# Performance work log

Hardware: AMD Instinct MI355X
Metric: run time of the kernel (lower is better)

The kernel has to match this reference:

```python
import jax, jax.numpy as jnp
import numpy as np
import math

B, C, T = 8, 256, 8192
G = 128          # group_size
QK = 128         # query_key_dim
HID = 512        # int(input_dim * expansion_factor)


def laplace_attn(x):
    mu = math.sqrt(0.5)
    std = math.sqrt(0.25 * math.pi)
    return (1.0 + jax.lax.erf((x - mu) / (std * math.sqrt(2.0)))) * 0.5


def setup_inputs() -> dict:
    key = jax.random.key(0)
    ks = jax.random.split(key, 12)
    s = 0.02
    q = jax.random.normal(ks[0], (B, C, T), jnp.float32)
    k = jax.random.normal(ks[1], (B, C, T), jnp.float32)
    v = jax.random.normal(ks[2], (B, C, T), jnp.float32)
    masks = jax.random.randint(ks[3], (B, 1, T), 0, 2).astype(jnp.float32)
    Wg = jax.random.normal(ks[4], (C, HID), jnp.float32) * s
    bg = jnp.zeros((HID,), jnp.float32)
    Wv = jax.random.normal(ks[5], (C, HID), jnp.float32) * s
    bv = jnp.zeros((HID,), jnp.float32)
    Wqk = jax.random.normal(ks[6], (C, QK), jnp.float32) * s
    bqk = jnp.zeros((QK,), jnp.float32)
    gamma = 1.0 + jax.random.normal(ks[7], (4, QK), jnp.float32) * s
    beta = jnp.zeros((4, QK), jnp.float32)
    Wo = jax.random.normal(ks[8], (HID, C), jnp.float32) * s
    bo = jnp.zeros((C,), jnp.float32)
    return {"q": q, "k": k, "v": v, "masks": masks,
            "Wg": Wg, "bg": bg, "Wv": Wv, "bv": bv,
            "Wqk": Wqk, "bqk": bqk, "gamma": gamma, "beta": beta,
            "Wo": Wo, "bo": bo}


def reference(q, k, v, masks, Wg, bg, Wv, bv, Wqk, bqk, gamma, beta, Wo, bo):
    # gen_key_padding_mask: batches whose mask is all-zero are reset to 1
    all_zero = jnp.sum(masks, axis=(1, 2)) == 0.0            # [B]
    masks = jnp.where(all_zero[:, None, None], 1.0, masks)    # [B,1,T]
    kpm = masks[:, 0, :] == 0.0                                # [B,T] True where mask==0

    # InstanceNorm1d (no affine): normalize q over the T axis per (b, c)
    mu = jnp.mean(q, axis=-1, keepdims=True)
    var = jnp.var(q, axis=-1, keepdims=True)
    qn = (q - mu) / jnp.sqrt(var + 1e-5)

    x = jnp.transpose(qn, (0, 2, 1))   # [B,T,C]
    vt = jnp.transpose(v, (0, 2, 1))   # [B,T,C]

    gate = jax.nn.silu(x @ Wg + bg)    # [B,T,HID]
    vh = jax.nn.silu(vt @ Wv + bv)     # [B,T,HID]
    qk = jax.nn.silu(x @ Wqk + bqk)    # [B,T,QK]

    # OffsetScale with 4 heads -> quad_q, lin_q, quad_k, lin_k
    qk4 = qk[..., None, :] * gamma + beta              # [B,T,4,QK]
    quad_q, lin_q, quad_k, lin_k = (qk4[..., i, :] for i in range(4))

    # masked_fill(~lin_mask, 0): zero lin_k where kpm is False (source semantics)
    lin_k = jnp.where(kpm[..., None], lin_k, 0.0)

    # T is a multiple of G, so padding_to_multiple_of(n, g) == 0
    ng = T // G
    grp = lambda t: t.reshape(B, ng, G, t.shape[-1])
    qq, lq, qkk, lk, vg = map(grp, (quad_q, lin_q, quad_k, lin_k, vh))
    kpm_g = kpm.reshape(B, ng, 1, G)                   # [B,g,1,j]

    # quadratic (local, per-group) attention
    sim = jnp.einsum('bgid,bgjd->bgij', qq, qkk) / G
    attn = laplace_attn(sim)
    attn = jnp.where(kpm_g, attn, 0.0)                 # masked_fill(~kpm, 0)
    quad_out = jnp.einsum('bgij,bgje->bgie', attn, vg)

    # linear (global) attention, non-causal, per-group context
    lin_kv = jnp.einsum('bgnd,bgne->bgde', lk, vg) / T
    lin_out = jnp.einsum('bgnd,bgde->bgne', lq, lin_kv)

    out = gate * (quad_out + lin_out).reshape(B, T, HID)
    out = (out @ Wo + bo).transpose(0, 2, 1)           # [B,C,T]
    return out * masks
```

## Files before the change

### kernel.cpp

```cpp
#include <hip/hip_runtime.h>
#include <stdint.h>

#define B_ 8
#define C_ 256
#define T_ 8192
#define G_ 128
#define QK_ 128
#define HID_ 512
#define NG_ 64

typedef __attribute__((ext_vector_type(8))) short bf16x8;
typedef __attribute__((ext_vector_type(4))) short s16x4;
typedef __attribute__((ext_vector_type(4))) float f32x4;

__device__ __forceinline__ float b2f(short s){
  union { float f; unsigned u; } v; v.u = ((unsigned)(unsigned short)s) << 16; return v.f;
}
__device__ __forceinline__ short f2b(float f){
  union { float f; unsigned u; } v; v.f = f;
  unsigned r = (v.u + 0x7FFFu + ((v.u >> 16) & 1u)) >> 16;
  return (short)r;
}
__device__ __forceinline__ float silu_f(float x){ return x / (1.0f + expf(-x)); }
__device__ __forceinline__ float laplace_f(float x){
  return 0.5f * (1.0f + erff((x - 0.70710678f) * 0.79788456f));
}
__device__ __forceinline__ f32x4 mfma16(bf16x8 a, bf16x8 b, f32x4 c){
  return __builtin_amdgcn_mfma_f32_16x16x32_bf16(a, b, c, 0, 0, 0);
}

__global__ void kw(const float* __restrict__ Wg, const float* __restrict__ Wv,
                   const float* __restrict__ Wqk, const float* __restrict__ Wo,
                   short* __restrict__ wgT, short* __restrict__ wvT,
                   short* __restrict__ wqkT, short* __restrict__ woT){
  int idx = blockIdx.x * 256 + threadIdx.x;
  int stride = gridDim.x * 256;
  for (int i = idx; i < C_ * HID_; i += stride){
    int c = i / HID_, e = i % HID_;
    wgT[e * C_ + c] = f2b(Wg[i]);
    wvT[e * C_ + c] = f2b(Wv[i]);
  }
  for (int i = idx; i < C_ * QK_; i += stride){
    int c = i / QK_, d = i % QK_;
    wqkT[d * C_ + c] = f2b(Wqk[i]);
  }
  for (int i = idx; i < HID_ * C_; i += stride){
    int e = i / C_, c = i % C_;
    woT[c * HID_ + e] = f2b(Wo[i]);
  }
}

__global__ void k0(const float* __restrict__ masks, float* __restrict__ m_eff,
                   float* __restrict__ kpmf){
  int b = blockIdx.x, tid = threadIdx.x;
  __shared__ float red[256];
  float s = 0.f;
  for (int t = tid; t < T_; t += 256) s += masks[b * T_ + t];
  red[tid] = s; __syncthreads();
  for (int k = 128; k > 0; k >>= 1){ if (tid < k) red[tid] += red[tid + k]; __syncthreads(); }
  bool az = (red[0] == 0.0f);
  for (int t = tid; t < T_; t += 256){
    float m = az ? 1.0f : masks[b * T_ + t];
    m_eff[b * T_ + t] = m;
    kpmf[b * T_ + t] = (m == 0.0f) ? 1.0f : 0.0f;
  }
}

__global__ void k1(const float* __restrict__ q, float* __restrict__ mu, float* __restrict__ rstd){
  int bc = blockIdx.x, tid = threadIdx.x;
  const float* row = q + (size_t)bc * T_;
  float s = 0.f, ss = 0.f;
  for (int t = tid * 4; t < T_; t += 256 * 4){
    float4 v = *(const float4*)(row + t);
    s += v.x + v.y + v.z + v.w;
    ss += v.x * v.x + v.y * v.y + v.z * v.z + v.w * v.w;
  }
  __shared__ float r1[256], r2[256];
  r1[tid] = s; r2[tid] = ss; __syncthreads();
  for (int k = 128; k > 0; k >>= 1){
    if (tid < k){ r1[tid] += r1[tid + k]; r2[tid] += r2[tid + k]; }
    __syncthreads();
  }
  if (tid == 0){
    float m = r1[0] / (float)T_;
    float var = r2[0] / (float)T_ - m * m;
    mu[bc] = m;
    rstd[bc] = rsqrtf(var + 1e-5f);
  }
}

__launch_bounds__(512)
__global__ void k2(const float* __restrict__ q, const float* __restrict__ v,
                   const float* __restrict__ mu, const float* __restrict__ rstd,
                   const short* __restrict__ wgT, const short* __restrict__ wvT,
                   const short* __restrict__ wqkT,
                   const float* __restrict__ bg, const float* __restrict__ bqk,
                   const float* __restrict__ bv,
                   const float* __restrict__ gamma, const float* __restrict__ beta,
                   const float* __restrict__ kpmf,
                   short* __restrict__ qqb, short* __restrict__ lqb,
                   short* __restrict__ qkkb, short* __restrict__ lkb,
                   short* __restrict__ gate, short* __restrict__ vhT){
  __shared__ __align__(16) short xlds[64 * 264];
  __shared__ __align__(16) short stage[9728];
  int blk = blockIdx.x;
  int b = blk >> 7, tile = blk & 127;
  int t0 = tile * 64;
  int tid = threadIdx.x;
  int w = tid >> 6, lane = tid & 63, lr = lane & 15, lg = lane >> 4;
  int wm = w >> 2, wn = w & 3;
  int i0w = wm * 32, n0w = wn * 32;

  {
    int cr = tid >> 4, tf = (tid & 15) * 4;
    #pragma unroll
    for (int it = 0; it < 8; ++it){
      int c = it * 32 + cr;
      float4 val = *(const float4*)(q + (size_t)(b * C_ + c) * T_ + t0 + tf);
      float m = mu[b * C_ + c], rs = rstd[b * C_ + c];
      xlds[(tf + 0) * 264 + c] = f2b((val.x - m) * rs);
      xlds[(tf + 1) * 264 + c] = f2b((val.y - m) * rs);
      xlds[(tf + 2) * 264 + c] = f2b((val.z - m) * rs);
      xlds[(tf + 3) * 264 + c] = f2b((val.w - m) * rs);
    }
  }
  __syncthreads();

  for (int p = 0; p < 5; ++p){
    const short* wt = (p < 4) ? (wgT + p * 128 * C_) : wqkT;
    const float* bias = (p < 4) ? (bg + p * 128) : bqk;
    f32x4 acc[2][2];
    #pragma unroll
    for (int mi = 0; mi < 2; ++mi)
      #pragma unroll
      for (int ni = 0; ni < 2; ++ni) acc[mi][ni] = (f32x4){0.f, 0.f, 0.f, 0.f};
    #pragma unroll
    for (int ks = 0; ks < 8; ++ks){
      int kb = ks * 32 + lg * 8;
      bf16x8 a[2], bb[2];
      #pragma unroll
      for (int mi = 0; mi < 2; ++mi)
        a[mi] = *(const bf16x8*)&xlds[(i0w + mi * 16 + lr) * 264 + kb];
      #pragma unroll
      for (int ni = 0; ni < 2; ++ni)
        bb[ni] = *(const bf16x8*)(wt + (n0w + ni * 16 + lr) * C_ + kb);
      #pragma unroll
      for (int mi = 0; mi < 2; ++mi)
        #pragma unroll
        for (int ni = 0; ni < 2; ++ni)
          acc[mi][ni] = mfma16(a[mi], bb[ni], acc[mi][ni]);
    }
    if (p < 4){
      #pragma unroll
      for (int ni = 0; ni < 2; ++ni){
        float bvv = bias[n0w + ni * 16 + lr];
        #pragma unroll
        for (int mi = 0; mi < 2; ++mi)
          #pragma unroll
          for (int r = 0; r < 4; ++r){
            int i = i0w + mi * 16 + lg * 4 + r;
            stage[i * 136 + n0w + ni * 16 + lr] = f2b(silu_f(acc[mi][ni][r] + bvv));
          }
      }
      __syncthreads();
      int row = tid >> 3, l8 = tid & 7;
      short* dst = gate + (size_t)(b * T_ + t0 + row) * HID_ + p * 128 + l8 * 16;
      *(uint4*)(dst) = *(const uint4*)&stage[row * 136 + l8 * 16];
      *(uint4*)(dst + 8) = *(const uint4*)&stage[row * 136 + l8 * 16 + 8];
      __syncthreads();
    } else {
      float sreg[2][2][4];
      float kpv[2][4];
      #pragma unroll
      for (int ni = 0; ni < 2; ++ni){
        float bvv = bias[n0w + ni * 16 + lr];
        #pragma unroll
        for (int mi = 0; mi < 2; ++mi)
          #pragma unroll
          for (int r = 0; r < 4; ++r)
            sreg[mi][ni][r] = silu_f(acc[mi][ni][r] + bvv);
      }
      #pragma unroll
      for (int mi = 0; mi < 2; ++mi)
        #pragma unroll
        for (int r = 0; r < 4; ++r)
          kpv[mi][r] = kpmf[b * T_ + t0 + i0w + mi * 16 + lg * 4 + r];
      short* hd[4] = {qqb, lqb, qkkb, lkb};
      for (int h = 0; h < 4; ++h){
        float gv[2], bvv2[2];
        #pragma unroll
        for (int ni = 0; ni < 2; ++ni){
          int n = n0w + ni * 16 + lr;
          gv[ni] = gamma[h * QK_ + n];
          bvv2[ni] = beta[h * QK_ + n];
        }
        #pragma unroll
        for (int mi = 0; mi < 2; ++mi)
          #pragma unroll
          for (int ni = 0; ni < 2; ++ni)
            #pragma unroll
            for (int r = 0; r < 4; ++r){
              float val = sreg[mi][ni][r] * gv[ni] + bvv2[ni];
              if (h == 3) val *= kpv[mi][r];
              stage[(i0w + mi * 16 + lg * 4 + r) * 136 + n0w + ni * 16 + lr] = f2b(val);
            }
        __syncthreads();
        int row = tid >> 3, l8 = tid & 7;
        short* dst = hd[h] + (size_t)(b * T_ + t0 + row) * QK_ + l8 * 16;
        *(uint4*)(dst) = *(const uint4*)&stage[row * 136 + l8 * 16];
        *(uint4*)(dst + 8) = *(const uint4*)&stage[row * 136 + l8 * 16 + 8];
        __syncthreads();
      }
    }
  }

  {
    int cr = tid >> 4, tf = (tid & 15) * 4;
    #pragma unroll
    for (int it = 0; it < 8; ++it){
      int c = it * 32 + cr;
      float4 val = *(const float4*)(v + (size_t)(b * C_ + c) * T_ + t0 + tf);
      xlds[(tf + 0) * 264 + c] = f2b(val.x);
      xlds[(tf + 1) * 264 + c] = f2b(val.y);
      xlds[(tf + 2) * 264 + c] = f2b(val.z);
      xlds[(tf + 3) * 264 + c] = f2b(val.w);
    }
  }
  __syncthreads();
  for (int p = 0; p < 4; ++p){
    const short* wt = wvT + p * 128 * C_;
    f32x4 acc[2][2];
    #pragma unroll
    for (int mi = 0; mi < 2; ++mi)
      #pragma unroll
      for (int ni = 0; ni < 2; ++ni) acc[mi][ni] = (f32x4){0.f, 0.f, 0.f, 0.f};
    #pragma unroll
    for (int ks = 0; ks < 8; ++ks){
      int kb = ks * 32 + lg * 8;
      bf16x8 a[2], bb[2];
      #pragma unroll
      for (int mi = 0; mi < 2; ++mi)
        a[mi] = *(const bf16x8*)&xlds[(i0w + mi * 16 + lr) * 264 + kb];
      #pragma unroll
      for (int ni = 0; ni < 2; ++ni)
        bb[ni] = *(const bf16x8*)(wt + (n0w + ni * 16 + lr) * C_ + kb);
      #pragma unroll
      for (int mi = 0; mi < 2; ++mi)
        #pragma unroll
        for (int ni = 0; ni < 2; ++ni)
          acc[mi][ni] = mfma16(a[mi], bb[ni], acc[mi][ni]);
    }
    #pragma unroll
    for (int ni = 0; ni < 2; ++ni){
      int n = n0w + ni * 16 + lr;
      float bvv = bv[p * 128 + n];
      #pragma unroll
      for (int mi = 0; mi < 2; ++mi){
        int ib = i0w + mi * 16 + lg * 4;
        s16x4 pk;
        #pragma unroll
        for (int r = 0; r < 4; ++r) pk[r] = f2b(silu_f(acc[mi][ni][r] + bvv));
        *(s16x4*)&stage[n * 72 + ib] = pk;
      }
    }
    __syncthreads();
    int row = tid >> 2, l4 = tid & 3;
    short* dst = vhT + (size_t)(b * HID_ + p * 128 + row) * T_ + t0 + l4 * 16;
    *(uint4*)(dst) = *(const uint4*)&stage[row * 72 + l4 * 16];
    *(uint4*)(dst + 8) = *(const uint4*)&stage[row * 72 + l4 * 16 + 8];
    __syncthreads();
  }
}

__launch_bounds__(512)
__global__ void k3(const short* __restrict__ qqb, const short* __restrict__ qkkb,
                   const short* __restrict__ lqb, const short* __restrict__ lkb,
                   const short* __restrict__ gate, const short* __restrict__ vhT,
                   const short* __restrict__ woT,
                   const float* __restrict__ kpmf, const float* __restrict__ m_eff,
                   const float* __restrict__ bo, float* __restrict__ out){
  __shared__ __align__(16) short slotA[128 * 136];
  __shared__ __align__(16) short slotB[128 * 136];
  __shared__ __align__(16) short slotC[128 * 136];
  int blk = blockIdx.x;
  int b = blk >> 6, grp = blk & 63;
  int t0 = grp * G_;
  int tid = threadIdx.x;
  int w = tid >> 6, lane = tid & 63, lr = lane & 15, lg = lane >> 4;
  int wm = w >> 2, wn = w & 3;
  int i0w = wm * 64;
  int j0w = wn * 32;
  int e0w = wn * 32;
  int d0w = wn * 32;
  int c0w = wn * 64;

  {
    const short* src = lkb + (size_t)(b * T_ + t0) * QK_;
    int d4 = (tid & 31) * 4;
    #pragma unroll
    for (int rep = 0; rep < 8; ++rep){
      int n = rep * 16 + (tid >> 5);
      s16x4 vv = *(const s16x4*)(src + n * QK_ + d4);
      #pragma unroll
      for (int r = 0; r < 4; ++r) slotC[(d4 + r) * 136 + n] = vv[r];
    }
  }

  {
    const short* qqp = qqb + (size_t)(b * T_ + t0) * QK_;
    const short* qkkp = qkkb + (size_t)(b * T_ + t0) * QK_;
    f32x4 sacc[4][2];
    #pragma unroll
    for (int mi = 0; mi < 4; ++mi)
      #pragma unroll
      for (int ni = 0; ni < 2; ++ni) sacc[mi][ni] = (f32x4){0.f, 0.f, 0.f, 0.f};
    #pragma unroll
    for (int ks = 0; ks < 4; ++ks){
      int kb = ks * 32 + lg * 8;
      bf16x8 a[4], bb[2];
      #pragma unroll
      for (int mi = 0; mi < 4; ++mi)
        a[mi] = *(const bf16x8*)(qqp + (i0w + mi * 16 + lr) * QK_ + kb);
      #pragma unroll
      for (int ni = 0; ni < 2; ++ni)
        bb[ni] = *(const bf16x8*)(qkkp + (j0w + ni * 16 + lr) * QK_ + kb);
      #pragma unroll
      for (int mi = 0; mi < 4; ++mi)
        #pragma unroll
        for (int ni = 0; ni < 2; ++ni)
          sacc[mi][ni] = mfma16(a[mi], bb[ni], sacc[mi][ni]);
    }
    #pragma unroll
    for (int ni = 0; ni < 2; ++ni){
      int j = j0w + ni * 16 + lr;
      float kp = kpmf[b * T_ + t0 + j];
      #pragma unroll
      for (int mi = 0; mi < 4; ++mi)
        #pragma unroll
        for (int r = 0; r < 4; ++r){
          int i = i0w + mi * 16 + lg * 4 + r;
          float s = sacc[mi][ni][r] * (1.0f / 128.0f);
          slotB[i * 136 + j] = f2b(laplace_f(s) * kp);
        }
    }
  }
  __syncthreads();

  f32x4 oacc[4][4];
  #pragma unroll
  for (int mi = 0; mi < 4; ++mi)
    #pragma unroll
    for (int ni = 0; ni < 4; ++ni) oacc[mi][ni] = (f32x4){0.f, 0.f, 0.f, 0.f};

  const short* lqp = lqb + (size_t)(b * T_ + t0) * QK_;

  for (int cN = 0; cN < 4; ++cN){
    int e0 = cN * 128;
    const short* vhp = vhT + (size_t)(b * HID_ + e0) * T_ + t0;

    f32x4 pacc[4][2];
    #pragma unroll
    for (int mi = 0; mi < 4; ++mi)
      #pragma unroll
      for (int ni = 0; ni < 2; ++ni) pacc[mi][ni] = (f32x4){0.f, 0.f, 0.f, 0.f};
    #pragma unroll
    for (int ks = 0; ks < 4; ++ks){
      int jb = ks * 32 + lg * 8;
      bf16x8 a[4], bb[2];
      #pragma unroll
      for (int mi = 0; mi < 4; ++mi)
        a[mi] = *(const bf16x8*)&slotB[(i0w + mi * 16 + lr) * 136 + jb];
      #pragma unroll
      for (int ni = 0; ni < 2; ++ni)
        bb[ni] = *(const bf16x8*)(vhp + (size_t)(e0w + ni * 16 + lr) * T_ + jb);
      #pragma unroll
      for (int mi = 0; mi < 4; ++mi)
        #pragma unroll
        for (int ni = 0; ni < 2; ++ni)
          pacc[mi][ni] = mfma16(a[mi], bb[ni], pacc[mi][ni]);
    }

    {
      f32x4 lacc[4][2];
      #pragma unroll
      for (int mi = 0; mi < 4; ++mi)
        #pragma unroll
        for (int ni = 0; ni < 2; ++ni) lacc[mi][ni] = (f32x4){0.f, 0.f, 0.f, 0.f};
      #pragma unroll
      for (int ks = 0; ks < 4; ++ks){
        int jb = ks * 32 + lg * 8;
        bf16x8 a[4], bb[2];
        #pragma unroll
        for (int mi = 0; mi < 4; ++mi)
          a[mi] = *(const bf16x8*)(vhp + (size_t)(i0w + mi * 16 + lr) * T_ + jb);
        #pragma unroll
        for (int ni = 0; ni < 2; ++ni)
          bb[ni] = *(const bf16x8*)&slotC[(d0w + ni * 16 + lr) * 136 + jb];
        #pragma unroll
        for (int mi = 0; mi < 4; ++mi)
          #pragma unroll
          for (int ni = 0; ni < 2; ++ni)
            lacc[mi][ni] = mfma16(a[mi], bb[ni], lacc[mi][ni]);
      }
      #pragma unroll
      for (int mi = 0; mi < 4; ++mi)
        #pragma unroll
        for (int ni = 0; ni < 2; ++ni){
          int d = d0w + ni * 16 + lr;
          #pragma unroll
          for (int r = 0; r < 4; ++r){
            int e = i0w + mi * 16 + lg * 4 + r;
            slotA[e * 136 + d] = f2b(lacc[mi][ni][r] * (1.0f / 8192.0f));
          }
        }
    }
    __syncthreads();

    #pragma unroll
    for (int ks = 0; ks < 4; ++ks){
      int db = ks * 32 + lg * 8;
      bf16x8 a[4], bb[2];
      #pragma unroll
      for (int mi = 0; mi < 4; ++mi)
        a[mi] = *(const bf16x8*)(lqp + (i0w + mi * 16 + lr) * QK_ + db);
      #pragma unroll
      for (int ni = 0; ni < 2; ++ni)
        bb[ni] = *(const bf16x8*)&slotA[(e0w + ni * 16 + lr) * 136 + db];
      #pragma unroll
      for (int mi = 0; mi < 4; ++mi)
        #pragma unroll
        for (int ni = 0; ni < 2; ++ni)
          pacc[mi][ni] = mfma16(a[mi], bb[ni], pacc[mi][ni]);
    }
    __syncthreads();

    {
      const short* gp = gate + (size_t)(b * T_ + t0) * HID_ + e0;
      int row = tid >> 2, l4 = tid & 3;
      #pragma unroll
      for (int jj = 0; jj < 4; ++jj)
        *(uint4*)&slotA[row * 136 + l4 * 32 + jj * 8] =
            *(const uint4*)(gp + (size_t)row * HID_ + l4 * 32 + jj * 8);
    }
    __syncthreads();

    #pragma unroll
    for (int mi = 0; mi < 4; ++mi)
      #pragma unroll
      for (int ni = 0; ni < 2; ++ni){
        int e = e0w + ni * 16 + lr;
        #pragma unroll
        for (int r = 0; r < 4; ++r){
          int i = i0w + mi * 16 + lg * 4 + r;
          int idx = i * 136 + e;
          slotA[idx] = f2b(b2f(slotA[idx]) * pacc[mi][ni][r]);
        }
      }
    __syncthreads();

    #pragma unroll
    for (int ks = 0; ks < 4; ++ks){
      int eb = ks * 32 + lg * 8;
      bf16x8 a[4], bb[4];
      #pragma unroll
      for (int mi = 0; mi < 4; ++mi)
        a[mi] = *(const bf16x8*)&slotA[(i0w + mi * 16 + lr) * 136 + eb];
      #pragma unroll
      for (int ni = 0; ni < 4; ++ni)
        bb[ni] = *(const bf16x8*)(woT + (size_t)(c0w + ni * 16 + lr) * HID_ + e0 + eb);
      #pragma unroll
      for (int mi = 0; mi < 4; ++mi)
        #pragma unroll
        for (int ni = 0; ni < 4; ++ni)
          oacc[mi][ni] = mfma16(a[mi], bb[ni], oacc[mi][ni]);
    }
    __syncthreads();
  }

  float* fstage = (float*)(void*)slotA;
  for (int cp = 0; cp < 4; ++cp){
    if (wn == cp){
      #pragma unroll
      for (int mi = 0; mi < 4; ++mi)
        #pragma unroll
        for (int ni = 0; ni < 4; ++ni){
          int cc = ni * 16 + lr;
          int ib = i0w + mi * 16 + lg * 4;
          *(f32x4*)&fstage[cc * 132 + ib] = oacc[mi][ni];
        }
    }
    __syncthreads();
    int crow = tid >> 3, l8 = tid & 7;
    int c = cp * 64 + crow;
    float bov = bo[c];
    float* orow = out + (size_t)(b * C_ + c) * T_ + t0;
    const float* mrow = m_eff + (size_t)b * T_ + t0;
    #pragma unroll
    for (int jj = 0; jj < 4; ++jj){
      int toff = l8 * 16 + jj * 4;
      float4 a = *(const float4*)&fstage[crow * 132 + toff];
      float4 m = *(const float4*)(mrow + toff);
      float4 o;
      o.x = (a.x + bov) * m.x; o.y = (a.y + bov) * m.y;
      o.z = (a.z + bov) * m.z; o.w = (a.w + bov) * m.w;
      *(float4*)(orow + toff) = o;
    }
    __syncthreads();
  }
}

extern "C" void kernel_launch(void* const* d_in, const int* in_sizes, int n_in,
                              void* d_out, int out_size, void* d_ws, size_t ws_size,
                              hipStream_t stream) {
  const float* q     = (const float*)d_in[0];
  const float* v     = (const float*)d_in[2];
  const float* masks = (const float*)d_in[3];
  const float* Wg    = (const float*)d_in[4];
  const float* bg    = (const float*)d_in[5];
  const float* Wv    = (const float*)d_in[6];
  const float* bv    = (const float*)d_in[7];
  const float* Wqk   = (const float*)d_in[8];
  const float* bqk   = (const float*)d_in[9];
  const float* gamma = (const float*)d_in[10];
  const float* beta  = (const float*)d_in[11];
  const float* Wo    = (const float*)d_in[12];
  const float* bo    = (const float*)d_in[13];
  float* out = (float*)d_out;

  char* ws = (char*)d_ws;
  size_t o = 0;
  auto nxt = [&](size_t bytes) -> char* {
    char* p = ws + o;
    o += (bytes + 255) & ~(size_t)255;
    return p;
  };
  short* wgT   = (short*)nxt((size_t)HID_ * C_ * 2);
  short* wvT   = (short*)nxt((size_t)HID_ * C_ * 2);
  short* wqkT  = (short*)nxt((size_t)QK_ * C_ * 2);
  short* woT   = (short*)nxt((size_t)C_ * HID_ * 2);
  float* muW   = (float*)nxt((size_t)B_ * C_ * 4);
  float* rstdW = (float*)nxt((size_t)B_ * C_ * 4);
  float* m_eff = (float*)nxt((size_t)B_ * T_ * 4);
  float* kpmf  = (float*)nxt((size_t)B_ * T_ * 4);
  short* qqb   = (short*)nxt((size_t)B_ * T_ * QK_ * 2);
  short* lqb   = (short*)nxt((size_t)B_ * T_ * QK_ * 2);
  short* qkkb  = (short*)nxt((size_t)B_ * T_ * QK_ * 2);
  short* lkb   = (short*)nxt((size_t)B_ * T_ * QK_ * 2);
  short* gateW = (short*)nxt((size_t)B_ * T_ * HID_ * 2);
  short* vhT   = (short*)nxt((size_t)B_ * HID_ * T_ * 2);
  (void)in_sizes; (void)n_in; (void)out_size; (void)ws_size;

  kw<<<dim3(512), dim3(256), 0, stream>>>(Wg, Wv, Wqk, Wo, wgT, wvT, wqkT, woT);
  k0<<<dim3(B_), dim3(256), 0, stream>>>(masks, m_eff, kpmf);
  k1<<<dim3(B_ * C_), dim3(256), 0, stream>>>(q, muW, rstdW);
  k2<<<dim3(B_ * (T_ / 64)), dim3(512), 0, stream>>>(q, v, muW, rstdW, wgT, wvT, wqkT,
                                                     bg, bqk, bv, gamma, beta, kpmf,
                                                     qqb, lqb, qkkb, lkb, gateW, vhT);
  k3<<<dim3(B_ * NG_), dim3(512), 0, stream>>>(qqb, qkkb, lqb, lkb, gateW, vhT, woT,
                                               kpmf, m_eff, bo, out);
}
```

Baseline: 563.5 us.

## Split projection kernel into transpose pre-pass and 128-row projection kernels

Replaces the monolithic projection kernel with three kernels. kA normalizes q and converts q and v to bf16 in time-major layout. kB computes gate and qk with 128-row tiles and writes lin_k already transposed. kC computes the v projection into vhT, which reuses the xT workspace. Because lin_k arrives pre-transposed, the attention kernel no longer needs its LDS staging buffer, which cuts its shared-memory footprint, and silu switches to the fast __expf. The cost is an extra round trip of the bf16 transposed q/v through global memory, extra launches, and large LDS use per block in kB/kC.

Result: slower. 630.7 us (+11.9%).

```diff
diff --git a/kernel.cpp b/kernel.cpp
--- a/kernel.cpp
+++ b/kernel.cpp
@@ -21,7 +21,7 @@
   unsigned r = (v.u + 0x7FFFu + ((v.u >> 16) & 1u)) >> 16;
   return (short)r;
 }
-__device__ __forceinline__ float silu_f(float x){ return x / (1.0f + expf(-x)); }
+__device__ __forceinline__ float silu_f(float x){ return x / (1.0f + __expf(-x)); }
 __device__ __forceinline__ float laplace_f(float x){
   return 0.5f * (1.0f + erff((x - 0.70710678f) * 0.79788456f));
 }
@@ -89,199 +89,323 @@
   }
 }
 
+__global__ void kA(const float* __restrict__ q, const float* __restrict__ v,
+                   const float* __restrict__ mu, const float* __restrict__ rstd,
+                   short* __restrict__ xT, short* __restrict__ vT){
+  __shared__ __align__(16) short lds[64 * 72];
+  int blk = blockIdx.x;
+  int b = blk >> 9;
+  int rem = blk & 511;
+  int t0 = (rem >> 2) * 64;
+  int c0 = (rem & 3) * 64;
+  int tid = threadIdx.x;
+  int f = (tid & 15) * 4;
+  int crb = tid >> 4;
+
+  #pragma unroll
+  for (int it = 0; it < 4; ++it){
+    int cr = crb + it * 16;
+    int gc = b * C_ + c0 + cr;
+    float4 val = *(const float4*)(q + (size_t)gc * T_ + t0 + f);
+    float m = mu[gc], rs = rstd[gc];
+    lds[(f + 0) * 72 + cr] = f2b((val.x - m) * rs);
+    lds[(f + 1) * 72 + cr] = f2b((val.y - m) * rs);
+    lds[(f + 2) * 72 + cr] = f2b((val.z - m) * rs);
+    lds[(f + 3) * 72 + cr] = f2b((val.w - m) * rs);
+  }
+  __syncthreads();
+  {
+    int t = tid >> 2, l4 = tid & 3;
+    *(uint4*)(xT + (size_t)(b * T_ + t0 + t) * C_ + c0 + l4 * 16) =
+        *(const uint4*)&lds[t * 72 + l4 * 16];
+    *(uint4*)(xT + (size_t)(b * T_ + t0 + t) * C_ + c0 + l4 * 16 + 8) =
+        *(const uint4*)&lds[t * 72 + l4 * 16 + 8];
+  }
+  __syncthreads();
+
+  #pragma unroll
+  for (int it = 0; it < 4; ++it){
+    int cr = crb + it * 16;
+    int gc = b * C_ + c0 + cr;
+    float4 val = *(const float4*)(v + (size_t)gc * T_ + t0 + f);
+    lds[(f + 0) * 72 + cr] = f2b(val.x);
+    lds[(f + 1) * 72 + cr] = f2b(val.y);
+    lds[(f + 2) * 72 + cr] = f2b(val.z);
+    lds[(f + 3) * 72 + cr] = f2b(val.w);
+  }
+  __syncthreads();
+  {
+    int t = tid >> 2, l4 = tid & 3;
+    *(uint4*)(vT + (size_t)(b * T_ + t0 + t) * C_ + c0 + l4 * 16) =
+        *(const uint4*)&lds[t * 72 + l4 * 16];
+    *(uint4*)(vT + (size_t)(b * T_ + t0 + t) * C_ + c0 + l4 * 16 + 8) =
+        *(const uint4*)&lds[t * 72 + l4 * 16 + 8];
+  }
+}
+
 __launch_bounds__(512)
-__global__ void k2(const float* __restrict__ q, const float* __restrict__ v,
-                   const float* __restrict__ mu, const float* __restrict__ rstd,
-                   const short* __restrict__ wgT, const short* __restrict__ wvT,
-                   const short* __restrict__ wqkT,
+__global__ void kB(const short* __restrict__ xT,
+                   const short* __restrict__ wgT, const short* __restrict__ wqkT,
                    const float* __restrict__ bg, const float* __restrict__ bqk,
-                   const float* __restrict__ bv,
                    const float* __restrict__ gamma, const float* __restrict__ beta,
                    const float* __restrict__ kpmf,
+                   short* __restrict__ gate,
                    short* __restrict__ qqb, short* __restrict__ lqb,
-                   short* __restrict__ qkkb, short* __restrict__ lkb,
-                   short* __restrict__ gate, short* __restrict__ vhT){
-  __shared__ __align__(16) short xlds[64 * 264];
-  __shared__ __align__(16) short stage[9728];
+                   short* __restrict__ qkkb, short* __restrict__ lkT){
+  __shared__ __align__(16) short xs[128 * 264];
+  __shared__ __align__(16) short st[128 * 136];
   int blk = blockIdx.x;
-  int b = blk >> 7, tile = blk & 127;
-  int t0 = tile * 64;
+  int b = blk >> 6, tile = blk & 63;
+  int t0 = tile * 128;
   int tid = threadIdx.x;
   int w = tid >> 6, lane = tid & 63, lr = lane & 15, lg = lane >> 4;
   int wm = w >> 2, wn = w & 3;
-  int i0w = wm * 32, n0w = wn * 32;
+  int m0 = wm * 64, n0 = wn * 32;
 
   {
-    int cr = tid >> 4, tf = (tid & 15) * 4;
-    #pragma unroll
-    for (int it = 0; it < 8; ++it){
-      int c = it * 32 + cr;
-      float4 val = *(const float4*)(q + (size_t)(b * C_ + c) * T_ + t0 + tf);
-      float m = mu[b * C_ + c], rs = rstd[b * C_ + c];
-      xlds[(tf + 0) * 264 + c] = f2b((val.x - m) * rs);
-      xlds[(tf + 1) * 264 + c] = f2b((val.y - m) * rs);
-      xlds[(tf + 2) * 264 + c] = f2b((val.z - m) * rs);
-      xlds[(tf + 3) * 264 + c] = f2b((val.w - m) * rs);
+    const short* src = xT + (size_t)(b * T_ + t0) * C_;
+    int r = tid >> 4, c16 = (tid & 15) * 16;
+    #pragma unroll
+    for (int it = 0; it < 4; ++it){
+      int row = r + it * 32;
+      *(uint4*)&xs[row * 264 + c16]     = *(const uint4*)(src + (size_t)row * C_ + c16);
+      *(uint4*)&xs[row * 264 + c16 + 8] = *(const uint4*)(src + (size_t)row * C_ + c16 + 8);
     }
   }
   __syncthreads();
 
-  for (int p = 0; p < 5; ++p){
-    const short* wt = (p < 4) ? (wgT + p * 128 * C_) : wqkT;
-    const float* bias = (p < 4) ? (bg + p * 128) : bqk;
-    f32x4 acc[2][2];
-    #pragma unroll
-    for (int mi = 0; mi < 2; ++mi)
+  for (int p = 0; p < 4; ++p){
+    f32x4 acc[4][2];
+    #pragma unroll
+    for (int mi = 0; mi < 4; ++mi)
       #pragma unroll
       for (int ni = 0; ni < 2; ++ni) acc[mi][ni] = (f32x4){0.f, 0.f, 0.f, 0.f};
     #pragma unroll
     for (int ks = 0; ks < 8; ++ks){
       int kb = ks * 32 + lg * 8;
-      bf16x8 a[2], bb[2];
-      #pragma unroll
-      for (int mi = 0; mi < 2; ++mi)
-        a[mi] = *(const bf16x8*)&xlds[(i0w + mi * 16 + lr) * 264 + kb];
+      bf16x8 a[4], bb[2];
+      #pragma unroll
+      for (int mi = 0; mi < 4; ++mi)
+        a[mi] = *(const bf16x8*)&xs[(m0 + mi * 16 + lr) * 264 + kb];
       #pragma unroll
       for (int ni = 0; ni < 2; ++ni)
-        bb[ni] = *(const bf16x8*)(wt + (n0w + ni * 16 + lr) * C_ + kb);
-      #pragma unroll
-      for (int mi = 0; mi < 2; ++mi)
+        bb[ni] = *(const bf16x8*)(wgT + (size_t)(p * 128 + n0 + ni * 16 + lr) * C_ + kb);
+      #pragma unroll
+      for (int mi = 0; mi < 4; ++mi)
         #pragma unroll
         for (int ni = 0; ni < 2; ++ni)
           acc[mi][ni] = mfma16(a[mi], bb[ni], acc[mi][ni]);
     }
-    if (p < 4){
+    #pragma unroll
+    for (int ni = 0; ni < 2; ++ni){
+      int e = p * 128 + n0 + ni * 16 + lr;
+      float bvv = bg[e];
+      #pragma unroll
+      for (int mi = 0; mi < 4; ++mi)
+        #pragma unroll
+        for (int r = 0; r < 4; ++r)
+          st[(m0 + mi * 16 + lg * 4 + r) * 136 + n0 + ni * 16 + lr] =
+              f2b(silu_f(acc[mi][ni][r] + bvv));
+    }
+    __syncthreads();
+    {
+      int row = tid >> 2, l4 = tid & 3;
+      short* dst = gate + (size_t)(b * T_ + t0 + row) * HID_ + p * 128 + l4 * 32;
+      const short* srcs = &st[row * 136 + l4 * 32];
+      #pragma unroll
+      for (int jj = 0; jj < 4; ++jj)
+        *(uint4*)(dst + jj * 8) = *(const uint4*)(srcs + jj * 8);
+    }
+    __syncthreads();
+  }
+
+  {
+    f32x4 acc[4][2];
+    #pragma unroll
+    for (int mi = 0; mi < 4; ++mi)
+      #pragma unroll
+      for (int ni = 0; ni < 2; ++ni) acc[mi][ni] = (f32x4){0.f, 0.f, 0.f, 0.f};
+    #pragma unroll
+    for (int ks = 0; ks < 8; ++ks){
+      int kb = ks * 32 + lg * 8;
+      bf16x8 a[4], bb[2];
+      #pragma unroll
+      for (int mi = 0; mi < 4; ++mi)
+        a[mi] = *(const bf16x8*)&xs[(m0 + mi * 16 + lr) * 264 + kb];
+      #pragma unroll
+      for (int ni = 0; ni < 2; ++ni)
+        bb[ni] = *(const bf16x8*)(wqkT + (size_t)(n0 + ni * 16 + lr) * C_ + kb);
+      #pragma unroll
+      for (int mi = 0; mi < 4; ++mi)
+        #pragma unroll
+        for (int ni = 0; ni < 2; ++ni)
+          acc[mi][ni] = mfma16(a[mi], bb[ni], acc[mi][ni]);
+    }
+    float sreg[4][2][4];
+    #pragma unroll
+    for (int ni = 0; ni < 2; ++ni){
+      float bvv = bqk[n0 + ni * 16 + lr];
+      #pragma unroll
+      for (int mi = 0; mi < 4; ++mi)
+        #pragma unroll
+        for (int r = 0; r < 4; ++r)
+          sreg[mi][ni][r] = silu_f(acc[mi][ni][r] + bvv);
+    }
+    short* hd[3] = {qqb, lqb, qkkb};
+    for (int h = 0; h < 3; ++h){
       #pragma unroll
       for (int ni = 0; ni < 2; ++ni){
-        float bvv = bias[n0w + ni * 16 + lr];
-        #pragma unroll
-        for (int mi = 0; mi < 2; ++mi)
+        int d = n0 + ni * 16 + lr;
+        float gv = gamma[h * QK_ + d], bt = beta[h * QK_ + d];
+        #pragma unroll
+        for (int mi = 0; mi < 4; ++mi)
           #pragma unroll
-          for (int r = 0; r < 4; ++r){
-            int i = i0w + mi * 16 + lg * 4 + r;
-            stage[i * 136 + n0w + ni * 16 + lr] = f2b(silu_f(acc[mi][ni][r] + bvv));
-          }
+          for (int r = 0; r < 4; ++r)
+            st[(m0 + mi * 16 + lg * 4 + r) * 136 + d] = f2b(sreg[mi][ni][r] * gv + bt);
       }
       __syncthreads();
-      int row = tid >> 3, l8 = tid & 7;
-      short* dst = gate + (size_t)(b * T_ + t0 + row) * HID_ + p * 128 + l8 * 16;
-      *(uint4*)(dst) = *(const uint4*)&stage[row * 136 + l8 * 16];
-      *(uint4*)(dst + 8) = *(const uint4*)&stage[row * 136 + l8 * 16 + 8];
+      {
+        int row = tid >> 2, l4 = tid & 3;
+        short* dst = hd[h] + (size_t)(b * T_ + t0 + row) * QK_ + l4 * 32;
+        const short* srcs = &st[row * 136 + l4 * 32];
+        #pragma unroll
+        for (int jj = 0; jj < 4; ++jj)
+          *(uint4*)(dst + jj * 8) = *(const uint4*)(srcs + jj * 8);
+      }
       __syncthreads();
-    } else {
-      float sreg[2][2][4];
-      float kpv[2][4];
-      #pragma unroll
-      for (int ni = 0; ni < 2; ++ni){
-        float bvv = bias[n0w + ni * 16 + lr];
-        #pragma unroll
-        for (int mi = 0; mi < 2; ++mi)
-          #pragma unroll
-          for (int r = 0; r < 4; ++r)
-            sreg[mi][ni][r] = silu_f(acc[mi][ni][r] + bvv);
-      }
-      #pragma unroll
-      for (int mi = 0; mi < 2; ++mi)
-        #pragma unroll
-        for (int r = 0; r < 4; ++r)
-          kpv[mi][r] = kpmf[b * T_ + t0 + i0w + mi * 16 + lg * 4 + r];
-      short* hd[4] = {qqb, lqb, qkkb, lkb};
-      for (int h = 0; h < 4; ++h){
-        float gv[2], bvv2[2];
-        #pragma unroll
-        for (int ni = 0; ni < 2; ++ni){
-          int n = n0w + ni * 16 + lr;
-          gv[ni] = gamma[h * QK_ + n];
-          bvv2[ni] = beta[h * QK_ + n];
-        }
-        #pragma unroll
-        for (int mi = 0; mi < 2; ++mi)
-          #pragma unroll
-          for (int ni = 0; ni < 2; ++ni)
-            #pragma unroll
-            for (int r = 0; r < 4; ++r){
-              float val = sreg[mi][ni][r] * gv[ni] + bvv2[ni];
-              if (h == 3) val *= kpv[mi][r];
-              stage[(i0w + mi * 16 + lg * 4 + r) * 136 + n0w + ni * 16 + lr] = f2b(val);
-            }
-        __syncthreads();
-        int row = tid >> 3, l8 = tid & 7;
-        short* dst = hd[h] + (size_t)(b * T_ + t0 + row) * QK_ + l8 * 16;
-        *(uint4*)(dst) = *(const uint4*)&stage[row * 136 + l8 * 16];
-        *(uint4*)(dst + 8) = *(const uint4*)&stage[row * 136 + l8 * 16 + 8];
-        __syncthreads();
-      }
     }
   }
 
   {
-    int cr = tid >> 4, tf = (tid & 15) * 4;
-    #pragma unroll
-    for (int it = 0; it < 8; ++it){
-      int c = it * 32 + cr;
-      float4 val = *(const float4*)(v + (size_t)(b * C_ + c) * T_ + t0 + tf);
-      xlds[(tf + 0) * 264 + c] = f2b(val.x);
-      xlds[(tf + 1) * 264 + c] = f2b(val.y);
-      xlds[(tf + 2) * 264 + c] = f2b(val.z);
-      xlds[(tf + 3) * 264 + c] = f2b(val.w);
-    }
-  }
-  __syncthreads();
-  for (int p = 0; p < 4; ++p){
-    const short* wt = wvT + p * 128 * C_;
-    f32x4 acc[2][2];
-    #pragma unroll
-    for (int mi = 0; mi < 2; ++mi)
+    f32x4 acc[4][2];
+    #pragma unroll
+    for (int mi = 0; mi < 4; ++mi)
       #pragma unroll
       for (int ni = 0; ni < 2; ++ni) acc[mi][ni] = (f32x4){0.f, 0.f, 0.f, 0.f};
     #pragma unroll
     for (int ks = 0; ks < 8; ++ks){
       int kb = ks * 32 + lg * 8;
-      bf16x8 a[2], bb[2];
-      #pragma unroll
-      for (int mi = 0; mi < 2; ++mi)
-        a[mi] = *(const bf16x8*)&xlds[(i0w + mi * 16 + lr) * 264 + kb];
+      bf16x8 a[4], bb[2];
+      #pragma unroll
+      for (int mi = 0; mi < 4; ++mi)
+        a[mi] = *(const bf16x8*)(wqkT + (size_t)(m0 + mi * 16 + lr) * C_ + kb);
       #pragma unroll
       for (int ni = 0; ni < 2; ++ni)
-        bb[ni] = *(const bf16x8*)(wt + (n0w + ni * 16 + lr) * C_ + kb);
-      #pragma unroll
-      for (int mi = 0; mi < 2; ++mi)
+        bb[ni] = *(const bf16x8*)&xs[(n0 + ni * 16 + lr) * 264 + kb];
+      #pragma unroll
+      for (int mi = 0; mi < 4; ++mi)
         #pragma unroll
         for (int ni = 0; ni < 2; ++ni)
           acc[mi][ni] = mfma16(a[mi], bb[ni], acc[mi][ni]);
     }
-    #pragma unroll
-    for (int ni = 0; ni < 2; ++ni){
-      int n = n0w + ni * 16 + lr;
-      float bvv = bv[p * 128 + n];
-      #pragma unroll
-      for (int mi = 0; mi < 2; ++mi){
-        int ib = i0w + mi * 16 + lg * 4;
-        s16x4 pk;
-        #pragma unroll
-        for (int r = 0; r < 4; ++r) pk[r] = f2b(silu_f(acc[mi][ni][r] + bvv));
-        *(s16x4*)&stage[n * 72 + ib] = pk;
+    float kp[2];
+    #pragma unroll
+    for (int ni = 0; ni < 2; ++ni)
+      kp[ni] = kpmf[b * T_ + t0 + n0 + ni * 16 + lr];
+    #pragma unroll
+    for (int mi = 0; mi < 4; ++mi)
+      #pragma unroll
+      for (int r = 0; r < 4; ++r){
+        int d = m0 + mi * 16 + lg * 4 + r;
+        float bvv = bqk[d];
+        float gv = gamma[3 * QK_ + d], bt = beta[3 * QK_ + d];
+        #pragma unroll
+        for (int ni = 0; ni < 2; ++ni){
+          float val = (silu_f(acc[mi][ni][r] + bvv) * gv + bt) * kp[ni];
+          st[d * 136 + n0 + ni * 16 + lr] = f2b(val);
+        }
       }
-    }
-    __syncthreads();
-    int row = tid >> 2, l4 = tid & 3;
-    short* dst = vhT + (size_t)(b * HID_ + p * 128 + row) * T_ + t0 + l4 * 16;
-    *(uint4*)(dst) = *(const uint4*)&stage[row * 72 + l4 * 16];
-    *(uint4*)(dst + 8) = *(const uint4*)&stage[row * 72 + l4 * 16 + 8];
+    __syncthreads();
+    {
+      int row = tid >> 2, l4 = tid & 3;
+      short* dst = lkT + (size_t)(b * QK_ + row) * T_ + t0 + l4 * 32;
+      const short* srcs = &st[row * 136 + l4 * 32];
+      #pragma unroll
+      for (int jj = 0; jj < 4; ++jj)
+        *(uint4*)(dst + jj * 8) = *(const uint4*)(srcs + jj * 8);
+    }
+  }
+}
+
+__launch_bounds__(512)
+__global__ void kC(const short* __restrict__ vT, const short* __restrict__ wvT,
+                   const float* __restrict__ bv, short* __restrict__ vhT){
+  __shared__ __align__(16) short vs[128 * 264];
+  __shared__ __align__(16) short st[128 * 136];
+  int blk = blockIdx.x;
+  int b = blk >> 6, tile = blk & 63;
+  int t0 = tile * 128;
+  int tid = threadIdx.x;
+  int w = tid >> 6, lane = tid & 63, lr = lane & 15, lg = lane >> 4;
+  int wm = w >> 2, wn = w & 3;
+  int m0 = wm * 64, n0 = wn * 32;
+
+  {
+    const short* src = vT + (size_t)(b * T_ + t0) * C_;
+    int r = tid >> 4, c16 = (tid & 15) * 16;
+    #pragma unroll
+    for (int it = 0; it < 4; ++it){
+      int row = r + it * 32;
+      *(uint4*)&vs[row * 264 + c16]     = *(const uint4*)(src + (size_t)row * C_ + c16);
+      *(uint4*)&vs[row * 264 + c16 + 8] = *(const uint4*)(src + (size_t)row * C_ + c16 + 8);
+    }
+  }
+  __syncthreads();
+
+  for (int p = 0; p < 4; ++p){
+    f32x4 acc[4][2];
+    #pragma unroll
+    for (int mi = 0; mi < 4; ++mi)
+      #pragma unroll
+      for (int ni = 0; ni < 2; ++ni) acc[mi][ni] = (f32x4){0.f, 0.f, 0.f, 0.f};
+    #pragma unroll
+    for (int ks = 0; ks < 8; ++ks){
+      int kb = ks * 32 + lg * 8;
+      bf16x8 a[4], bb[2];
+      #pragma unroll
+      for (int mi = 0; mi < 4; ++mi)
+        a[mi] = *(const bf16x8*)(wvT + (size_t)(p * 128 + m0 + mi * 16 + lr) * C_ + kb);
+      #pragma unroll
+      for (int ni = 0; ni < 2; ++ni)
+        bb[ni] = *(const bf16x8*)&vs[(n0 + ni * 16 + lr) * 264 + kb];
+      #pragma unroll
+      for (int mi = 0; mi < 4; ++mi)
+        #pragma unroll
+        for (int ni = 0; ni < 2; ++ni)
+          acc[mi][ni] = mfma16(a[mi], bb[ni], acc[mi][ni]);
+    }
+    #pragma unroll
+    for (int mi = 0; mi < 4; ++mi)
+      #pragma unroll
+      for (int r = 0; r < 4; ++r){
+        int el = m0 + mi * 16 + lg * 4 + r;
+        float bvv = bv[p * 128 + el];
+        #pragma unroll
+        for (int ni = 0; ni < 2; ++ni)
+          st[el * 136 + n0 + ni * 16 + lr] = f2b(silu_f(acc[mi][ni][r] + bvv));
+      }
+    __syncthreads();
+    {
+      int row = tid >> 2, l4 = tid & 3;
+      short* dst = vhT + (size_t)(b * HID_ + p * 128 + row) * T_ + t0 + l4 * 32;
+      const short* srcs = &st[row * 136 + l4 * 32];
+      #pragma unroll
+      for (int jj = 0; jj < 4; ++jj)
+        *(uint4*)(dst + jj * 8) = *(const uint4*)(srcs + jj * 8);
+    }
     __syncthreads();
   }
 }
 
 __launch_bounds__(512)
 __global__ void k3(const short* __restrict__ qqb, const short* __restrict__ qkkb,
-                   const short* __restrict__ lqb, const short* __restrict__ lkb,
+                   const short* __restrict__ lqb, const short* __restrict__ lkT,
                    const short* __restrict__ gate, const short* __restrict__ vhT,
                    const short* __restrict__ woT,
                    const float* __restrict__ kpmf, const float* __restrict__ m_eff,
                    const float* __restrict__ bo, float* __restrict__ out){
   __shared__ __align__(16) short slotA[128 * 136];
   __shared__ __align__(16) short slotB[128 * 136];
-  __shared__ __align__(16) short slotC[128 * 136];
   int blk = blockIdx.x;
   int b = blk >> 6, grp = blk & 63;
   int t0 = grp * G_;
@@ -295,18 +419,6 @@
   int c0w = wn * 64;
 
   {
-    const short* src = lkb + (size_t)(b * T_ + t0) * QK_;
-    int d4 = (tid & 31) * 4;
-    #pragma unroll
-    for (int rep = 0; rep < 8; ++rep){
-      int n = rep * 16 + (tid >> 5);
-      s16x4 vv = *(const s16x4*)(src + n * QK_ + d4);
-      #pragma unroll
-      for (int r = 0; r < 4; ++r) slotC[(d4 + r) * 136 + n] = vv[r];
-    }
-  }
-
-  {
     const short* qqp = qqb + (size_t)(b * T_ + t0) * QK_;
     const short* qkkp = qkkb + (size_t)(b * T_ + t0) * QK_;
     f32x4 sacc[4][2];
@@ -395,7 +507,7 @@
           a[mi] = *(const bf16x8*)(vhp + (size_t)(i0w + mi * 16 + lr) * T_ + jb);
         #pragma unroll
         for (int ni = 0; ni < 2; ++ni)
-          bb[ni] = *(const bf16x8*)&slotC[(d0w + ni * 16 + lr) * 136 + jb];
+          bb[ni] = *(const bf16x8*)(lkT + (size_t)(b * QK_ + d0w + ni * 16 + lr) * T_ + t0 + jb);
         #pragma unroll
         for (int mi = 0; mi < 4; ++mi)
           #pragma unroll
@@ -545,17 +657,21 @@
   short* qqb   = (short*)nxt((size_t)B_ * T_ * QK_ * 2);
   short* lqb   = (short*)nxt((size_t)B_ * T_ * QK_ * 2);
   short* qkkb  = (short*)nxt((size_t)B_ * T_ * QK_ * 2);
-  short* lkb   = (short*)nxt((size_t)B_ * T_ * QK_ * 2);
+  short* lkT   = (short*)nxt((size_t)B_ * QK_ * T_ * 2);
   short* gateW = (short*)nxt((size_t)B_ * T_ * HID_ * 2);
-  short* vhT   = (short*)nxt((size_t)B_ * HID_ * T_ * 2);
+  short* vTb   = (short*)nxt((size_t)B_ * T_ * C_ * 2);
+  short* xTb   = (short*)nxt((size_t)B_ * T_ * C_ * 2);
+  (void)nxt((size_t)B_ * T_ * C_ * 2);
+  short* vhT   = xTb;
   (void)in_sizes; (void)n_in; (void)out_size; (void)ws_size;
 
   kw<<<dim3(512), dim3(256), 0, stream>>>(Wg, Wv, Wqk, Wo, wgT, wvT, wqkT, woT);
   k0<<<dim3(B_), dim3(256), 0, stream>>>(masks, m_eff, kpmf);
   k1<<<dim3(B_ * C_), dim3(256), 0, stream>>>(q, muW, rstdW);
-  k2<<<dim3(B_ * (T_ / 64)), dim3(512), 0, stream>>>(q, v, muW, rstdW, wgT, wvT, wqkT,
-                                                     bg, bqk, bv, gamma, beta, kpmf,
-                                                     qqb, lqb, qkkb, lkb, gateW, vhT);
-  k3<<<dim3(B_ * NG_), dim3(512), 0, stream>>>(qqb, qkkb, lqb, lkb, gateW, vhT, woT,
+  kA<<<dim3(B_ * 512), dim3(256), 0, stream>>>(q, v, muW, rstdW, xTb, vTb);
+  kB<<<dim3(B_ * 64), dim3(512), 0, stream>>>(xTb, wgT, wqkT, bg, bqk, gamma, beta, kpmf,
+                                              gateW, qqb, lqb, qkkb, lkT);
+  kC<<<dim3(B_ * 64), dim3(512), 0, stream>>>(vTb, wvT, bv, vhT);
+  k3<<<dim3(B_ * NG_), dim3(512), 0, stream>>>(qqb, qkkb, lqb, lkT, gateW, vhT, woT,
                                                kpmf, m_eff, bo, out);
 }
```
